# Kernel optimization log

Measured on AMD Instinct MI355X. Metric: run time of the kernel, lower is better.

Reference implementation:

```python
import jax, jax.numpy as jnp
import numpy as np

N_VAR, N_CON, N_SOC = 100_000, 100_000, 20_000
E_VC, E_SC = 2_000_000, 300_000
H = 64


def setup_inputs() -> dict:
    key = jax.random.key(0)
    ks = iter(jax.random.split(key, 64))

    def rn(shape, s=0.05):
        return jax.random.normal(next(ks), shape, jnp.float32) * s

    inp = {
        "var_x": rn((N_VAR, 7), 1.0),
        "con_x": rn((N_CON, 4), 1.0),
        "soc_x": rn((N_SOC, 6), 1.0),
        "W_var": rn((7, H)), "b_var": jnp.zeros((H,), jnp.float32),
        "W_con": rn((4, H)), "b_con": jnp.zeros((H,), jnp.float32),
        "W_soc": rn((6, H)), "b_soc": jnp.zeros((H,), jnp.float32),
    }
    for l in ("l1", "l2"):
        for d in ("f", "b"):
            inp[f"{l}{d}_Wp"] = rn((H, H))
            inp[f"{l}{d}_bp"] = jnp.zeros((H,), jnp.float32)
            inp[f"{l}{d}_Ws"] = rn((H, H))
            inp[f"{l}{d}_Wn"] = rn((H, H))
            inp[f"{l}{d}_b"] = jnp.zeros((H,), jnp.float32)
    inp["W_hid"] = rn((H, H)); inp["b_hid"] = jnp.zeros((H,), jnp.float32)
    inp["W_out"] = rn((H, 1)); inp["b_out"] = jnp.zeros((1,), jnp.float32)
    inp["vc_src"] = jax.random.randint(next(ks), (E_VC,), 0, N_VAR)
    inp["vc_dst"] = jax.random.randint(next(ks), (E_VC,), 0, N_CON)
    inp["sc_src"] = jax.random.randint(next(ks), (E_SC,), 0, N_SOC)
    inp["sc_dst"] = jax.random.randint(next(ks), (E_SC,), 0, N_CON)
    return inp


def _sage_pool(x_src, x_dst, src, dst, n_dst, Wp, bp, Ws, Wn, b):
    """DGL SAGEConv(aggregator_type='pool') on one bipartite relation.

    max-pool of relu(fc_pool(src feats)) over in-edges, then fc_self + fc_neigh + bias.
    """
    pooled = jax.nn.relu(x_src @ Wp + bp)                       # [N_src, H]
    agg = jax.ops.segment_max(pooled[src], dst, num_segments=n_dst)  # [N_dst, H]
    agg = jnp.where(jnp.isfinite(agg), agg, 0.0)                # zero in-degree -> 0 (DGL semantics)
    return x_dst @ Ws + agg @ Wn + b


def reference(var_x, con_x, soc_x,
              W_var, b_var, W_con, b_con, W_soc, b_soc,
              l1f_Wp, l1f_bp, l1f_Ws, l1f_Wn, l1f_b,
              l1b_Wp, l1b_bp, l1b_Ws, l1b_Wn, l1b_b,
              l2f_Wp, l2f_bp, l2f_Ws, l2f_Wn, l2f_b,
              l2b_Wp, l2b_bp, l2b_Ws, l2b_Wn, l2b_b,
              W_hid, b_hid, W_out, b_out,
              vc_src, vc_dst, sc_src, sc_dst):
    n_var, n_con, n_soc = var_x.shape[0], con_x.shape[0], soc_x.shape[0]

    # PreNormLayer with beta=0, sigma=1 (non-trainable, no pretrain update) is identity.
    h_var = jax.nn.relu(var_x @ W_var + b_var)
    h_con = jax.nn.relu(con_x @ W_con + b_con)
    h_soc = jax.nn.relu(soc_x @ W_soc + b_soc)

    # Each conv layer shares one SAGEConv for {v2c, s2c} and one for {c2v, c2s}.
    layers = [
        ((l1f_Wp, l1f_bp, l1f_Ws, l1f_Wn, l1f_b), (l1b_Wp, l1b_bp, l1b_Ws, l1b_Wn, l1b_b)),
        ((l2f_Wp, l2f_bp, l2f_Ws, l2f_Wn, l2f_b), (l2b_Wp, l2b_bp, l2b_Ws, l2b_Wn, l2b_b)),
    ]

    # n_passes = 1
    # forward half-pass: update constraint nodes; HeteroGraphConv sums v2c and s2c outputs.
    for fwd, _ in layers:
        c = (_sage_pool(h_var, h_con, vc_src, vc_dst, n_con, *fwd)
             + _sage_pool(h_soc, h_con, sc_src, sc_dst, n_con, *fwd))
        h_con = jax.nn.relu(c)
    # backward half-pass: update var and soc nodes from constraints (c2v, c2s = reversed edges).
    for _, bwd in layers:
        v = _sage_pool(h_con, h_var, vc_dst, vc_src, n_var, *bwd)
        s = _sage_pool(h_con, h_soc, sc_dst, sc_src, n_soc, *bwd)
        h_var = jax.nn.relu(v)
        h_soc = jax.nn.relu(s)

    # Output MLP: [Linear, ReLU]*2 in the source duplicates ONE shared Linear module.
    z = h_var
    for _ in range(2):
        z = jax.nn.relu(z @ W_hid + b_hid)
    return z @ W_out + b_out  # [n_var, 1] per-variable logits (readout_op=None)
```

## Files before the change

kernel.cpp:

```cpp
#include <hip/hip_runtime.h>

#define NV 100000
#define NC 100000
#define NSOC 20000
#define NVS (NV + NSOC)
#define EVC 2000000
#define ESC 300000
#define H 64

constexpr int BSH = 7;
constexpr int NBMAX = 1024;
constexpr int EPB = 8192;

template<int K1, int NSEC, bool RELU, int TR>
__global__ __launch_bounds__(256) void gemm_lds(
    const float* X1, const float* __restrict__ W1,
    const float* __restrict__ X2, const float* __restrict__ W2,
    const float* __restrict__ bias, float* out,
    int N, float s1)
{
  __shared__ __align__(16) float sx1[TR * K1];
  __shared__ __align__(16) float sx2[NSEC ? TR * H : 4];

  const int n0 = blockIdx.x * TR;

  if constexpr ((K1 & 3) == 0) {
    const float4* X4 = reinterpret_cast<const float4*>(X1);
    float4* S4 = reinterpret_cast<float4*>(sx1);
    const long base4 = (long)n0 * K1 / 4;
    const long lim4 = (long)N * K1 / 4;
    for (int i = threadIdx.x; i < TR * K1 / 4; i += 256)
      S4[i] = (base4 + i < lim4) ? X4[base4 + i] : make_float4(0.f, 0.f, 0.f, 0.f);
  } else {
    const long base = (long)n0 * K1;
    const long lim = (long)N * K1;
    for (int i = threadIdx.x; i < TR * K1; i += 256)
      sx1[i] = (base + i < lim) ? X1[base + i] : 0.f;
  }
  if constexpr (NSEC) {
    const float4* X4 = reinterpret_cast<const float4*>(X2);
    float4* S4 = reinterpret_cast<float4*>(sx2);
    const long base4 = (long)n0 * H / 4;
    const long lim4 = (long)N * H / 4;
    for (int i = threadIdx.x; i < TR * H / 4; i += 256)
      S4[i] = (base4 + i < lim4) ? X4[base4 + i] : make_float4(0.f, 0.f, 0.f, 0.f);
  }
  __syncthreads();

  const int lane = threadIdx.x & 63;
  const int wv = threadIdx.x >> 6;

  float w1[K1];
#pragma unroll
  for (int k = 0; k < K1; ++k) w1[k] = W1[k * H + lane];
  float w2[NSEC ? H : 1];
  if constexpr (NSEC) {
#pragma unroll
    for (int k = 0; k < H; ++k) w2[k] = W2[k * H + lane];
  }
  const float bj = bias[lane];

  constexpr int RPW = TR / 4;
  const int r0 = wv * RPW;

  if constexpr (K1 == H) {
    for (int i = 0; i < RPW; i += 2) {
      const int na = n0 + r0 + i;
      if (na >= N) break;
      const bool wb = (na + 1) < N;

      const float4* xa = reinterpret_cast<const float4*>(sx1 + (r0 + i) * H);
      const float4* xb = reinterpret_cast<const float4*>(sx1 + (r0 + i + 1) * H);
      float a0 = 0.f, a1 = 0.f, a2 = 0.f, a3 = 0.f;
      float b0 = 0.f, b1 = 0.f, b2 = 0.f, b3 = 0.f;
#pragma unroll
      for (int k4 = 0; k4 < H / 4; ++k4) {
        const float4 va = xa[k4];
        const float4 vb = xb[k4];
        a0 = fmaf(va.x, w1[4 * k4 + 0], a0);
        b0 = fmaf(vb.x, w1[4 * k4 + 0], b0);
        a1 = fmaf(va.y, w1[4 * k4 + 1], a1);
        b1 = fmaf(vb.y, w1[4 * k4 + 1], b1);
        a2 = fmaf(va.z, w1[4 * k4 + 2], a2);
        b2 = fmaf(vb.z, w1[4 * k4 + 2], b2);
        a3 = fmaf(va.w, w1[4 * k4 + 3], a3);
        b3 = fmaf(vb.w, w1[4 * k4 + 3], b3);
      }
      float accA = s1 * (((a0 + a1) + (a2 + a3)) + bj);
      float accB = s1 * (((b0 + b1) + (b2 + b3)) + bj);

      if constexpr (NSEC) {
        const float4* ya = reinterpret_cast<const float4*>(sx2 + (r0 + i) * H);
        const float4* yb = reinterpret_cast<const float4*>(sx2 + (r0 + i + 1) * H);
        a0 = 0.f; a1 = 0.f; a2 = 0.f; a3 = 0.f;
        b0 = 0.f; b1 = 0.f; b2 = 0.f; b3 = 0.f;
#pragma unroll
        for (int k4 = 0; k4 < H / 4; ++k4) {
          const float4 va = ya[k4];
          const float4 vb = yb[k4];
          a0 = fmaf(va.x, w2[4 * k4 + 0], a0);
          b0 = fmaf(vb.x, w2[4 * k4 + 0], b0);
          a1 = fmaf(va.y, w2[4 * k4 + 1], a1);
          b1 = fmaf(vb.y, w2[4 * k4 + 1], b1);
          a2 = fmaf(va.z, w2[4 * k4 + 2], a2);
          b2 = fmaf(vb.z, w2[4 * k4 + 2], b2);
          a3 = fmaf(va.w, w2[4 * k4 + 3], a3);
          b3 = fmaf(vb.w, w2[4 * k4 + 3], b3);
        }
        accA += (a0 + a1) + (a2 + a3);
        accB += (b0 + b1) + (b2 + b3);
      }

      if constexpr (RELU) { accA = fmaxf(accA, 0.f); accB = fmaxf(accB, 0.f); }
      out[(size_t)na * H + lane] = accA;
      if (wb) out[(size_t)(na + 1) * H + lane] = accB;
    }
  } else {
    for (int i = 0; i < RPW; i += 2) {
      const int na = n0 + r0 + i;
      if (na >= N) break;
      const bool wb = (na + 1) < N;
      const float* xa = sx1 + (r0 + i) * K1;
      const float* xb = sx1 + (r0 + i + 1) * K1;
      float accA = 0.f, accB = 0.f;
#pragma unroll
      for (int k = 0; k < K1; ++k) {
        accA = fmaf(xa[k], w1[k], accA);
        accB = fmaf(xb[k], w1[k], accB);
      }
      accA = s1 * (accA + bj);
      accB = s1 * (accB + bj);
      if constexpr (RELU) { accA = fmaxf(accA, 0.f); accB = fmaxf(accB, 0.f); }
      out[(size_t)na * H + lane] = accA;
      if (wb) out[(size_t)(na + 1) * H + lane] = accB;
    }
  }
}

template<int TR>
__global__ __launch_bounds__(256) void dualgemm_k(
    const float* __restrict__ X, const float* __restrict__ Wa,
    const float* __restrict__ ba, const float* __restrict__ Wb,
    const float* __restrict__ bb, float* __restrict__ out, int N)
{
  __shared__ __align__(16) float sx[TR * H];
  const int n0 = blockIdx.x * TR;
  {
    const float4* X4 = reinterpret_cast<const float4*>(X);
    float4* S4 = reinterpret_cast<float4*>(sx);
    const long base4 = (long)n0 * (H / 4);
    const long lim4 = (long)N * (H / 4);
    for (int i = threadIdx.x; i < TR * H / 4; i += 256)
      S4[i] = (base4 + i < lim4) ? X4[base4 + i] : make_float4(0.f, 0.f, 0.f, 0.f);
  }
  __syncthreads();

  const int lane = threadIdx.x & 63;
  const int wv = threadIdx.x >> 6;
  float wA[H], wB[H];
#pragma unroll
  for (int k = 0; k < H; ++k) { wA[k] = Wa[k * H + lane]; wB[k] = Wb[k * H + lane]; }
  const float bja = ba[lane];
  const float bjb = bb[lane];

  constexpr int RPW = TR / 4;
  const int r0 = wv * RPW;
  for (int i = 0; i < RPW; i += 2) {
    const int na = n0 + r0 + i;
    if (na >= N) break;
    const bool hasB = (na + 1) < N;

    const float4* xa = reinterpret_cast<const float4*>(sx + (r0 + i) * H);
    const float4* xb = reinterpret_cast<const float4*>(sx + (r0 + i + 1) * H);
    float pa0 = 0.f, pa1 = 0.f, pa2 = 0.f, pa3 = 0.f;
    float pb0 = 0.f, pb1 = 0.f, pb2 = 0.f, pb3 = 0.f;
    float qa0 = 0.f, qa1 = 0.f, qa2 = 0.f, qa3 = 0.f;
    float qb0 = 0.f, qb1 = 0.f, qb2 = 0.f, qb3 = 0.f;
#pragma unroll
    for (int k4 = 0; k4 < H / 4; ++k4) {
      const float4 va = xa[k4];
      const float4 vb = xb[k4];
      pa0 = fmaf(va.x, wA[4 * k4 + 0], pa0);
      pb0 = fmaf(vb.x, wA[4 * k4 + 0], pb0);
      qa0 = fmaf(va.x, wB[4 * k4 + 0], qa0);
      qb0 = fmaf(vb.x, wB[4 * k4 + 0], qb0);
      pa1 = fmaf(va.y, wA[4 * k4 + 1], pa1);
      pb1 = fmaf(vb.y, wA[4 * k4 + 1], pb1);
      qa1 = fmaf(va.y, wB[4 * k4 + 1], qa1);
      qb1 = fmaf(vb.y, wB[4 * k4 + 1], qb1);
      pa2 = fmaf(va.z, wA[4 * k4 + 2], pa2);
      pb2 = fmaf(vb.z, wA[4 * k4 + 2], pb2);
      qa2 = fmaf(va.z, wB[4 * k4 + 2], qa2);
      qb2 = fmaf(vb.z, wB[4 * k4 + 2], qb2);
      pa3 = fmaf(va.w, wA[4 * k4 + 3], pa3);
      pb3 = fmaf(vb.w, wA[4 * k4 + 3], pb3);
      qa3 = fmaf(va.w, wB[4 * k4 + 3], qa3);
      qb3 = fmaf(vb.w, wB[4 * k4 + 3], qb3);
    }
    const float accAa = fmaxf((pa0 + pa1) + (pa2 + pa3) + bja, 0.f);
    const float accAb = fmaxf((qa0 + qa1) + (qa2 + qa3) + bjb, 0.f);
    out[(size_t)na * 128 + lane] = accAa;
    out[(size_t)na * 128 + 64 + lane] = accAb;
    if (hasB) {
      const float accBa = fmaxf((pb0 + pb1) + (pb2 + pb3) + bja, 0.f);
      const float accBb = fmaxf((qb0 + qb1) + (qb2 + qb3) + bjb, 0.f);
      out[(size_t)(na + 1) * 128 + lane] = accBa;
      out[(size_t)(na + 1) * 128 + 64 + lane] = accBb;
    }
  }
}

template<int TR>
__global__ __launch_bounds__(256) void mlp_k(
    const float* __restrict__ X, const float* __restrict__ W,
    const float* __restrict__ bh, const float* __restrict__ Wout,
    const float* __restrict__ bo, float* __restrict__ out, int N)
{
  __shared__ __align__(16) float sx[TR * H];
  __shared__ __align__(16) float sz[4][H];

  const int n0 = blockIdx.x * TR;
  {
    const float4* X4 = reinterpret_cast<const float4*>(X);
    float4* S4 = reinterpret_cast<float4*>(sx);
    const long base4 = (long)n0 * H / 4;
    const long lim4 = (long)N * H / 4;
    for (int i = threadIdx.x; i < TR * H / 4; i += 256)
      S4[i] = (base4 + i < lim4) ? X4[base4 + i] : make_float4(0.f, 0.f, 0.f, 0.f);
  }
  __syncthreads();

  const int lane = threadIdx.x & 63;
  const int wv = threadIdx.x >> 6;
  float w[H];
#pragma unroll
  for (int k = 0; k < H; ++k) w[k] = W[k * H + lane];
  const float bhl = bh[lane];
  const float wo = Wout[lane];
  const float bol = bo[0];

  constexpr int RPW = TR / 4;
  const int r0 = wv * RPW;
  for (int i = 0; i < RPW; ++i) {
    const int n = n0 + r0 + i;
    if (n >= N) break;
    const float4* x4 = reinterpret_cast<const float4*>(sx + (r0 + i) * H);
    float a0 = 0.f, a1 = 0.f, a2 = 0.f, a3 = 0.f;
#pragma unroll
    for (int k4 = 0; k4 < H / 4; ++k4) {
      const float4 v = x4[k4];
      a0 = fmaf(v.x, w[4 * k4 + 0], a0);
      a1 = fmaf(v.y, w[4 * k4 + 1], a1);
      a2 = fmaf(v.z, w[4 * k4 + 2], a2);
      a3 = fmaf(v.w, w[4 * k4 + 3], a3);
    }
    const float z1 = fmaxf((a0 + a1) + (a2 + a3) + bhl, 0.f);
    sz[wv][lane] = z1;
    const float4* z4 = reinterpret_cast<const float4*>(sz[wv]);
    a0 = 0.f; a1 = 0.f; a2 = 0.f; a3 = 0.f;
#pragma unroll
    for (int k4 = 0; k4 < H / 4; ++k4) {
      const float4 v = z4[k4];
      a0 = fmaf(v.x, w[4 * k4 + 0], a0);
      a1 = fmaf(v.y, w[4 * k4 + 1], a1);
      a2 = fmaf(v.z, w[4 * k4 + 2], a2);
      a3 = fmaf(v.w, w[4 * k4 + 3], a3);
    }
    const float z2 = fmaxf((a0 + a1) + (a2 + a3) + bhl, 0.f);
    float v = z2 * wo;
#pragma unroll
    for (int off = 32; off; off >>= 1) v += __shfl_down(v, off);
    if (lane == 0) out[n] = v + bol;
  }
}

__global__ __launch_bounds__(256) void bhist_k(const int* __restrict__ key,
                                               int* __restrict__ bcnt, int E, int nb) {
  __shared__ int h[NBMAX];
  for (int i = threadIdx.x; i < nb; i += 256) h[i] = 0;
  __syncthreads();
  const int base = blockIdx.x * EPB;
  for (int i = threadIdx.x; i < EPB; i += 256) {
    const int e = base + i;
    if (e < E) atomicAdd(&h[key[e] >> BSH], 1);
  }
  __syncthreads();
  for (int i = threadIdx.x; i < nb; i += 256)
    if (h[i]) atomicAdd(&bcnt[i], h[i]);
}

__global__ __launch_bounds__(1024) void bscan_k(const int* __restrict__ bcnt,
                                                int* __restrict__ bcur,
                                                int* __restrict__ sbase, int nb) {
  __shared__ int s[1024];
  const int t = threadIdx.x;
  const int v = (t < nb) ? bcnt[t] : 0;
  s[t] = v;
  __syncthreads();
  for (int off = 1; off < 1024; off <<= 1) {
    int x = (t >= off) ? s[t - off] : 0;
    __syncthreads();
    s[t] += x;
    __syncthreads();
  }
  if (t < nb) {
    const int ex = s[t] - v;
    bcur[t] = ex;
    sbase[t] = ex;
    if (t == nb - 1) sbase[nb] = s[t];
  }
}

__global__ __launch_bounds__(256) void bscatter_k(
    const int* __restrict__ key, const int* __restrict__ payload,
    int* __restrict__ bcur, int2* __restrict__ sorted, int E, int nb) {
  __shared__ int h[NBMAX];
  __shared__ int gb[NBMAX];
  __shared__ unsigned short lr[EPB];
  for (int i = threadIdx.x; i < nb; i += 256) h[i] = 0;
  __syncthreads();
  const int base = blockIdx.x * EPB;
  for (int i = threadIdx.x; i < EPB; i += 256) {
    const int e = base + i;
    if (e < E) lr[i] = (unsigned short)atomicAdd(&h[key[e] >> BSH], 1);
  }
  __syncthreads();
  for (int i = threadIdx.x; i < nb; i += 256)
    if (h[i]) gb[i] = atomicAdd(&bcur[i], h[i]);
  __syncthreads();
  for (int i = threadIdx.x; i < EPB; i += 256) {
    const int e = base + i;
    if (e < E) {
      const int k = key[e];
      sorted[gb[k >> BSH] + lr[i]] = make_int2(k, payload[e]);
    }
  }
}

__global__ __launch_bounds__(256) void bfinish_k(
    const int2* __restrict__ sorted, const int* __restrict__ sbase,
    int* __restrict__ rp, int* __restrict__ ei, int Nn) {
  __shared__ int cnt[128];
// ... 74 lines not shown
  m.w = fmaxf(m.w, __shfl_xor(m.w, 32));
  return m;
}

__global__ __launch_bounds__(256) void gather2f_k(
    const float4* __restrict__ t4,
    const int* __restrict__ rpCv, const int* __restrict__ eiCv,
    const int* __restrict__ rpCs, const int* __restrict__ eiCs,
    float4* __restrict__ agg1, float4* __restrict__ agg2, int N)
{
  const int lane = threadIdx.x & 63;
  const int g = lane >> 5, sub = lane & 31;
  const int n = __builtin_amdgcn_readfirstlane(blockIdx.x * 4 + (threadIdx.x >> 6));
  if (n >= N) return;
  const float4 a = gmax2_csr(t4, rpCv, eiCv, n, g, sub);
  const float4 b = gmax2_csr(t4 + (size_t)NV * 32, rpCs, eiCs, n, g, sub);
  const float4 r = make_float4(a.x + b.x, a.y + b.y, a.z + b.z, a.w + b.w);
  if (g == 0) {
    if (sub < 16) agg1[(size_t)n * 16 + sub] = r;
    else          agg2[(size_t)n * 16 + (sub - 16)] = r;
  }
}

__global__ __launch_bounds__(256) void gathervs2_k(
    const float4* __restrict__ t4,
    const int* __restrict__ rpV, const int* __restrict__ eiV,
    const int* __restrict__ rpS, const int* __restrict__ eiS,
    float4* __restrict__ agg1, float4* __restrict__ agg2)
{
  const int lane = threadIdx.x & 63;
  const int g = lane >> 5, sub = lane & 31;
  const int n = __builtin_amdgcn_readfirstlane(blockIdx.x * 4 + (threadIdx.x >> 6));
  if (n >= NVS) return;
  float4 m;
  if (n < NV) m = gmax2_csr(t4, rpV, eiV, n, g, sub);
  else        m = gmax2_csr(t4, rpS, eiS, n - NV, g, sub);
  if (g == 0) {
    if (sub < 16) agg1[(size_t)n * 16 + sub] = m;
    else          agg2[(size_t)n * 16 + (sub - 16)] = m;
  }
}

extern "C" void kernel_launch(void* const* d_in, const int* in_sizes, int n_in,
                              void* d_out, int out_size, void* d_ws, size_t ws_size,
                              hipStream_t stream) {
  const float* var_x = (const float*)d_in[0];
  const float* con_x = (const float*)d_in[1];
  const float* soc_x = (const float*)d_in[2];
  const float* W_var = (const float*)d_in[3];
  const float* b_var = (const float*)d_in[4];
  const float* W_con = (const float*)d_in[5];
  const float* b_con = (const float*)d_in[6];
  const float* W_soc = (const float*)d_in[7];
  const float* b_soc = (const float*)d_in[8];
  const float* L[4][5];
  for (int l = 0; l < 4; ++l)
    for (int p = 0; p < 5; ++p)
      L[l][p] = (const float*)d_in[9 + l * 5 + p];
  const float* W_hid = (const float*)d_in[29];
  const float* b_hid = (const float*)d_in[30];
  const float* W_out = (const float*)d_in[31];
  const float* b_out = (const float*)d_in[32];
  const int* vc_src = (const int*)d_in[33];
  const int* vc_dst = (const int*)d_in[34];
  const int* sc_src = (const int*)d_in[35];
  const int* sc_dst = (const int*)d_in[36];

  char* ws = (char*)d_ws;
  const size_t F_VS = (size_t)NVS * H * 4;
  const size_t F_C  = (size_t)NC * H * 4;
  float* hvs   = (float*)(ws);
  float* h_con = (float*)(ws + F_VS);
  float* bufA  = (float*)(ws + F_VS + F_C);
  float* bufB  = (float*)(ws + 3 * F_VS + F_C);
  int2*  sorted = (int2*)bufB;
  char* csr = ws + 3 * F_VS + 3 * F_C;
  int* rpCv = (int*)(csr);
  int* eiCv = rpCv + (NC + 1);
  int* rpCs = eiCv + EVC;
  int* eiCs = rpCs + (NC + 1);
  int* rpV  = eiCs + ESC;
  int* eiV  = rpV + (NV + 1);
  int* rpS  = eiV + EVC;
  int* eiS  = rpS + (NSOC + 1);
  int* aux  = eiS + ESC;
  int* bcnt[4];
  for (int i = 0; i < 4; ++i) bcnt[i] = aux + i * 1024;
  int* bcur  = aux + 4 * 1024;
  int* sbase = aux + 5 * 1024;

  constexpr int TR = 64;
  auto grid_l = [](int n) { return dim3((unsigned)((n + TR - 1) / TR)); };
  auto grid_w = [](int n) { return dim3((unsigned)((n + 3) / 4)); };
  auto grid_b = [](int e) { return dim3((unsigned)((e + EPB - 1) / EPB)); };
  const dim3 B(256);

  float* h_var = hvs;
  float* h_soc = hvs + (size_t)NV * H;

  hipMemsetAsync(aux, 0, 4 * 1024 * sizeof(int), stream);

  auto build_csr = [&](const int* key, const int* payload, int E, int Nn,
                       int* rp, int* ei, int bi) {
    const int nb = (Nn + (1 << BSH) - 1) >> BSH;
    bhist_k<<<grid_b(E), B, 0, stream>>>(key, bcnt[bi], E, nb);
    bscan_k<<<dim3(1), dim3(1024), 0, stream>>>(bcnt[bi], bcur, sbase, nb);
    bscatter_k<<<grid_b(E), B, 0, stream>>>(key, payload, bcur, sorted, E, nb);
    bfinish_k<<<dim3((unsigned)nb), B, 0, stream>>>(sorted, sbase, rp, ei, Nn);
  };

  build_csr(vc_dst, vc_src, EVC, NC, rpCv, eiCv, 0);
  build_csr(sc_dst, sc_src, ESC, NC, rpCs, eiCs, 1);
  build_csr(vc_src, vc_dst, EVC, NV, rpV, eiV, 2);
  build_csr(sc_src, sc_dst, ESC, NSOC, rpS, eiS, 3);

  gemm_lds<7, 0, true, TR><<<grid_l(NV), B, 0, stream>>>(var_x, W_var, nullptr, nullptr, b_var, h_var, NV, 1.f);
  gemm_lds<4, 0, true, TR><<<grid_l(NC), B, 0, stream>>>(con_x, W_con, nullptr, nullptr, b_con, h_con, NC, 1.f);
  gemm_lds<6, 0, true, TR><<<grid_l(NSOC), B, 0, stream>>>(soc_x, W_soc, nullptr, nullptr, b_soc, h_soc, NSOC, 1.f);

  float* agg1f = bufB;
  float* agg2f = bufB + (size_t)NC * H;
  dualgemm_k<TR><<<grid_l(NVS), B, 0, stream>>>(hvs, L[0][0], L[0][1], L[2][0], L[2][1], bufA, NVS);
  gather2f_k<<<grid_w(NC), B, 0, stream>>>((const float4*)bufA, rpCv, eiCv, rpCs, eiCs,
                                           (float4*)agg1f, (float4*)agg2f, NC);
  gemm_lds<64, 1, true, TR><<<grid_l(NC), B, 0, stream>>>(h_con, L[0][2], agg1f, L[0][3], L[0][4], h_con, NC, 2.f);
  gemm_lds<64, 1, true, TR><<<grid_l(NC), B, 0, stream>>>(h_con, L[2][2], agg2f, L[2][3], L[2][4], h_con, NC, 2.f);

  float* agg1b = bufA;
  float* agg2b = bufA + (size_t)NVS * H;
  dualgemm_k<TR><<<grid_l(NC), B, 0, stream>>>(h_con, L[1][0], L[1][1], L[3][0], L[3][1], bufB, NC);
  gathervs2_k<<<grid_w(NVS), B, 0, stream>>>((const float4*)bufB, rpV, eiV, rpS, eiS,
                                             (float4*)agg1b, (float4*)agg2b);
  gemm_lds<64, 1, true, TR><<<grid_l(NVS), B, 0, stream>>>(hvs, L[1][2], agg1b, L[1][3], L[1][4], hvs, NVS, 1.f);
  gemm_lds<64, 1, true, TR><<<grid_l(NVS), B, 0, stream>>>(hvs, L[3][2], agg2b, L[3][3], L[3][4], hvs, NVS, 1.f);

  mlp_k<TR><<<grid_l(NV), B, 0, stream>>>(hvs, W_hid, b_hid, W_out, b_out, (float*)d_out, NV);
}
```

Measured before the change: 832.6 us.

## Fuse embedding, layer updates and MLP into per-tile kernels; skip soc backward path

Replaces the separate GEMM launches with fused per-tile kernels. Embedding and both pool projections run in one kernel; the constraint embedding, both forward updates and the backward pool projections run in another; the variable updates and output MLP run in a third, keeping intermediates in LDS instead of global memory. It drops the soc-node backward update entirely, since the output depends only on var nodes. It also merges the two vc CSR builds into one histogram/scan/scatter pass. This cuts global traffic and launch count at the price of more registers and LDS per block, which may reduce occupancy.

```diff
diff --git a/kernel.cpp b/kernel.cpp
--- a/kernel.cpp
+++ b/kernel.cpp
@@ -11,273 +11,293 @@
 constexpr int BSH = 7;
 constexpr int NBMAX = 1024;
 constexpr int EPB = 8192;
-
-template<int K1, int NSEC, bool RELU, int TR>
-__global__ __launch_bounds__(256) void gemm_lds(
-    const float* X1, const float* __restrict__ W1,
-    const float* __restrict__ X2, const float* __restrict__ W2,
-    const float* __restrict__ bias, float* out,
-    int N, float s1)
-{
-  __shared__ __align__(16) float sx1[TR * K1];
-  __shared__ __align__(16) float sx2[NSEC ? TR * H : 4];
-
-  const int n0 = blockIdx.x * TR;
-
-  if constexpr ((K1 & 3) == 0) {
-    const float4* X4 = reinterpret_cast<const float4*>(X1);
-    float4* S4 = reinterpret_cast<float4*>(sx1);
-    const long base4 = (long)n0 * K1 / 4;
-    const long lim4 = (long)N * K1 / 4;
-    for (int i = threadIdx.x; i < TR * K1 / 4; i += 256)
-      S4[i] = (base4 + i < lim4) ? X4[base4 + i] : make_float4(0.f, 0.f, 0.f, 0.f);
-  } else {
-    const long base = (long)n0 * K1;
-    const long lim = (long)N * K1;
-    for (int i = threadIdx.x; i < TR * K1; i += 256)
-      sx1[i] = (base + i < lim) ? X1[base + i] : 0.f;
-  }
-  if constexpr (NSEC) {
-    const float4* X4 = reinterpret_cast<const float4*>(X2);
-    float4* S4 = reinterpret_cast<float4*>(sx2);
-    const long base4 = (long)n0 * H / 4;
-    const long lim4 = (long)N * H / 4;
-    for (int i = threadIdx.x; i < TR * H / 4; i += 256)
-      S4[i] = (base4 + i < lim4) ? X4[base4 + i] : make_float4(0.f, 0.f, 0.f, 0.f);
-  }
-  __syncthreads();
-
-  const int lane = threadIdx.x & 63;
-  const int wv = threadIdx.x >> 6;
-
-  float w1[K1];
-#pragma unroll
-  for (int k = 0; k < K1; ++k) w1[k] = W1[k * H + lane];
-  float w2[NSEC ? H : 1];
-  if constexpr (NSEC) {
-#pragma unroll
-    for (int k = 0; k < H; ++k) w2[k] = W2[k * H + lane];
-  }
+constexpr int TR = 64;
+
+__device__ __forceinline__ void stage_tile(const float* __restrict__ X, float* s,
+                                           int n0, int N, int tid) {
+  const float4* X4 = reinterpret_cast<const float4*>(X);
+  float4* S4 = reinterpret_cast<float4*>(s);
+  const long base4 = (long)n0 * (H / 4);
+  const long lim4 = (long)N * (H / 4);
+  for (int i = tid; i < TR * H / 4; i += 256)
+    S4[i] = (base4 + i < lim4) ? X4[base4 + i] : make_float4(0.f, 0.f, 0.f, 0.f);
+}
+
+__device__ __forceinline__ void apply_layer_inplace(
+    float* sh, const float* sa,
+    const float* __restrict__ Wself, const float* __restrict__ Wneigh,
+    const float* __restrict__ bias, int lane, int r0, float s1)
+{
+  float ws[H], wn[H];
+#pragma unroll
+  for (int k = 0; k < H; ++k) ws[k] = Wself[k * H + lane];
+#pragma unroll
+  for (int k = 0; k < H; ++k) wn[k] = Wneigh[k * H + lane];
   const float bj = bias[lane];
-
-  constexpr int RPW = TR / 4;
-  const int r0 = wv * RPW;
-
-  if constexpr (K1 == H) {
-    for (int i = 0; i < RPW; i += 2) {
-      const int na = n0 + r0 + i;
-      if (na >= N) break;
-      const bool wb = (na + 1) < N;
-
-      const float4* xa = reinterpret_cast<const float4*>(sx1 + (r0 + i) * H);
-      const float4* xb = reinterpret_cast<const float4*>(sx1 + (r0 + i + 1) * H);
-      float a0 = 0.f, a1 = 0.f, a2 = 0.f, a3 = 0.f;
-      float b0 = 0.f, b1 = 0.f, b2 = 0.f, b3 = 0.f;
-#pragma unroll
-      for (int k4 = 0; k4 < H / 4; ++k4) {
-        const float4 va = xa[k4];
-        const float4 vb = xb[k4];
-        a0 = fmaf(va.x, w1[4 * k4 + 0], a0);
-        b0 = fmaf(vb.x, w1[4 * k4 + 0], b0);
-        a1 = fmaf(va.y, w1[4 * k4 + 1], a1);
-        b1 = fmaf(vb.y, w1[4 * k4 + 1], b1);
-        a2 = fmaf(va.z, w1[4 * k4 + 2], a2);
-        b2 = fmaf(vb.z, w1[4 * k4 + 2], b2);
-        a3 = fmaf(va.w, w1[4 * k4 + 3], a3);
-        b3 = fmaf(vb.w, w1[4 * k4 + 3], b3);
-      }
-      float accA = s1 * (((a0 + a1) + (a2 + a3)) + bj);
-      float accB = s1 * (((b0 + b1) + (b2 + b3)) + bj);
-
-      if constexpr (NSEC) {
-        const float4* ya = reinterpret_cast<const float4*>(sx2 + (r0 + i) * H);
-        const float4* yb = reinterpret_cast<const float4*>(sx2 + (r0 + i + 1) * H);
-        a0 = 0.f; a1 = 0.f; a2 = 0.f; a3 = 0.f;
-        b0 = 0.f; b1 = 0.f; b2 = 0.f; b3 = 0.f;
-#pragma unroll
-        for (int k4 = 0; k4 < H / 4; ++k4) {
-          const float4 va = ya[k4];
-          const float4 vb = yb[k4];
-          a0 = fmaf(va.x, w2[4 * k4 + 0], a0);
-          b0 = fmaf(vb.x, w2[4 * k4 + 0], b0);
-          a1 = fmaf(va.y, w2[4 * k4 + 1], a1);
-          b1 = fmaf(vb.y, w2[4 * k4 + 1], b1);
-          a2 = fmaf(va.z, w2[4 * k4 + 2], a2);
-          b2 = fmaf(vb.z, w2[4 * k4 + 2], b2);
-          a3 = fmaf(va.w, w2[4 * k4 + 3], a3);
-          b3 = fmaf(vb.w, w2[4 * k4 + 3], b3);
-        }
-        accA += (a0 + a1) + (a2 + a3);
-        accB += (b0 + b1) + (b2 + b3);
-      }
-
-      if constexpr (RELU) { accA = fmaxf(accA, 0.f); accB = fmaxf(accB, 0.f); }
-      out[(size_t)na * H + lane] = accA;
-      if (wb) out[(size_t)(na + 1) * H + lane] = accB;
-    }
-  } else {
-    for (int i = 0; i < RPW; i += 2) {
-      const int na = n0 + r0 + i;
-      if (na >= N) break;
-      const bool wb = (na + 1) < N;
-      const float* xa = sx1 + (r0 + i) * K1;
-      const float* xb = sx1 + (r0 + i + 1) * K1;
-      float accA = 0.f, accB = 0.f;
-#pragma unroll
-      for (int k = 0; k < K1; ++k) {
-        accA = fmaf(xa[k], w1[k], accA);
-        accB = fmaf(xb[k], w1[k], accB);
-      }
-      accA = s1 * (accA + bj);
-      accB = s1 * (accB + bj);
-      if constexpr (RELU) { accA = fmaxf(accA, 0.f); accB = fmaxf(accB, 0.f); }
-      out[(size_t)na * H + lane] = accA;
-      if (wb) out[(size_t)(na + 1) * H + lane] = accB;
-    }
-  }
-}
-
-template<int TR>
-__global__ __launch_bounds__(256) void dualgemm_k(
-    const float* __restrict__ X, const float* __restrict__ Wa,
-    const float* __restrict__ ba, const float* __restrict__ Wb,
-    const float* __restrict__ bb, float* __restrict__ out, int N)
-{
-  __shared__ __align__(16) float sx[TR * H];
+  for (int i = 0; i < 16; i += 2) {
+    const float4* xa = reinterpret_cast<const float4*>(sh + (r0 + i) * H);
+    const float4* xb = reinterpret_cast<const float4*>(sh + (r0 + i + 1) * H);
+    float a0 = 0.f, a1 = 0.f, a2 = 0.f, a3 = 0.f;
+    float b0 = 0.f, b1 = 0.f, b2 = 0.f, b3 = 0.f;
+#pragma unroll
+    for (int k4 = 0; k4 < H / 4; ++k4) {
+      const float4 va = xa[k4], vb = xb[k4];
+      a0 = fmaf(va.x, ws[4 * k4 + 0], a0); b0 = fmaf(vb.x, ws[4 * k4 + 0], b0);
+      a1 = fmaf(va.y, ws[4 * k4 + 1], a1); b1 = fmaf(vb.y, ws[4 * k4 + 1], b1);
+      a2 = fmaf(va.z, ws[4 * k4 + 2], a2); b2 = fmaf(vb.z, ws[4 * k4 + 2], b2);
+      a3 = fmaf(va.w, ws[4 * k4 + 3], a3); b3 = fmaf(vb.w, ws[4 * k4 + 3], b3);
+    }
+    float accA = s1 * (((a0 + a1) + (a2 + a3)) + bj);
+    float accB = s1 * (((b0 + b1) + (b2 + b3)) + bj);
+    const float4* ya = reinterpret_cast<const float4*>(sa + (r0 + i) * H);
+    const float4* yb = reinterpret_cast<const float4*>(sa + (r0 + i + 1) * H);
+    a0 = 0.f; a1 = 0.f; a2 = 0.f; a3 = 0.f;
+    b0 = 0.f; b1 = 0.f; b2 = 0.f; b3 = 0.f;
+#pragma unroll
+    for (int k4 = 0; k4 < H / 4; ++k4) {
+      const float4 va = ya[k4], vb = yb[k4];
+      a0 = fmaf(va.x, wn[4 * k4 + 0], a0); b0 = fmaf(vb.x, wn[4 * k4 + 0], b0);
+      a1 = fmaf(va.y, wn[4 * k4 + 1], a1); b1 = fmaf(vb.y, wn[4 * k4 + 1], b1);
+      a2 = fmaf(va.z, wn[4 * k4 + 2], a2); b2 = fmaf(vb.z, wn[4 * k4 + 2], b2);
+      a3 = fmaf(va.w, wn[4 * k4 + 3], a3); b3 = fmaf(vb.w, wn[4 * k4 + 3], b3);
+    }
+    accA += (a0 + a1) + (a2 + a3);
+    accB += (b0 + b1) + (b2 + b3);
+    sh[(r0 + i) * H + lane] = fmaxf(accA, 0.f);
+    sh[(r0 + i + 1) * H + lane] = fmaxf(accB, 0.f);
+  }
+}
+
+__device__ __forceinline__ void apply_lin_inplace(
+    float* sh, const float* __restrict__ W, const float* __restrict__ b,
+    int lane, int r0)
+{
+  float w[H];
+#pragma unroll
+  for (int k = 0; k < H; ++k) w[k] = W[k * H + lane];
+  const float bj = b[lane];
+  for (int i = 0; i < 16; i += 2) {
+    const float4* xa = reinterpret_cast<const float4*>(sh + (r0 + i) * H);
+    const float4* xb = reinterpret_cast<const float4*>(sh + (r0 + i + 1) * H);
+    float a0 = 0.f, a1 = 0.f, a2 = 0.f, a3 = 0.f;
+    float b0 = 0.f, b1 = 0.f, b2 = 0.f, b3 = 0.f;
+#pragma unroll
+    for (int k4 = 0; k4 < H / 4; ++k4) {
+      const float4 va = xa[k4], vb = xb[k4];
+      a0 = fmaf(va.x, w[4 * k4 + 0], a0); b0 = fmaf(vb.x, w[4 * k4 + 0], b0);
+      a1 = fmaf(va.y, w[4 * k4 + 1], a1); b1 = fmaf(vb.y, w[4 * k4 + 1], b1);
+      a2 = fmaf(va.z, w[4 * k4 + 2], a2); b2 = fmaf(vb.z, w[4 * k4 + 2], b2);
+      a3 = fmaf(va.w, w[4 * k4 + 3], a3); b3 = fmaf(vb.w, w[4 * k4 + 3], b3);
+    }
+    sh[(r0 + i) * H + lane] = fmaxf((a0 + a1) + (a2 + a3) + bj, 0.f);
+    sh[(r0 + i + 1) * H + lane] = fmaxf((b0 + b1) + (b2 + b3) + bj, 0.f);
+  }
+}
+
+__device__ __forceinline__ void apply_pool_out(
+    const float* sh, const float* __restrict__ Wp, const float* __restrict__ bp,
+    int lane, int r0, int n0, int N, float* __restrict__ pooled, int colOff)
+{
+  float w[H];
+#pragma unroll
+  for (int k = 0; k < H; ++k) w[k] = Wp[k * H + lane];
+  const float bj = bp[lane];
+  for (int i = 0; i < 16; i += 2) {
+    const float4* xa = reinterpret_cast<const float4*>(sh + (r0 + i) * H);
+    const float4* xb = reinterpret_cast<const float4*>(sh + (r0 + i + 1) * H);
+    float a0 = 0.f, a1 = 0.f, a2 = 0.f, a3 = 0.f;
+    float b0 = 0.f, b1 = 0.f, b2 = 0.f, b3 = 0.f;
+#pragma unroll
+    for (int k4 = 0; k4 < H / 4; ++k4) {
+      const float4 va = xa[k4], vb = xb[k4];
+      a0 = fmaf(va.x, w[4 * k4 + 0], a0); b0 = fmaf(vb.x, w[4 * k4 + 0], b0);
+      a1 = fmaf(va.y, w[4 * k4 + 1], a1); b1 = fmaf(vb.y, w[4 * k4 + 1], b1);
+      a2 = fmaf(va.z, w[4 * k4 + 2], a2); b2 = fmaf(vb.z, w[4 * k4 + 2], b2);
+      a3 = fmaf(va.w, w[4 * k4 + 3], a3); b3 = fmaf(vb.w, w[4 * k4 + 3], b3);
+    }
+    const int na = n0 + r0 + i;
+    if (na < N)
+      pooled[(size_t)na * 128 + colOff + lane] =
+          fmaxf((a0 + a1) + (a2 + a3) + bj, 0.f);
+    if (na + 1 < N)
+      pooled[(size_t)(na + 1) * 128 + colOff + lane] =
+          fmaxf((b0 + b1) + (b2 + b3) + bj, 0.f);
+  }
+}
+
+template<int K, bool WRITEH>
+__global__ __launch_bounds__(256) void emb_pool_k(
+    const float* __restrict__ X, const float* __restrict__ We,
+    const float* __restrict__ be,
+    const float* __restrict__ Wp1, const float* __restrict__ bp1,
+    const float* __restrict__ Wp2, const float* __restrict__ bp2,
+    float* __restrict__ h_out, float* __restrict__ pooled, int N)
+{
+  __shared__ __align__(16) float sxe[TR * K];
+  __shared__ __align__(16) float sh[TR * H];
   const int n0 = blockIdx.x * TR;
   {
-    const float4* X4 = reinterpret_cast<const float4*>(X);
-    float4* S4 = reinterpret_cast<float4*>(sx);
-    const long base4 = (long)n0 * (H / 4);
-    const long lim4 = (long)N * (H / 4);
-    for (int i = threadIdx.x; i < TR * H / 4; i += 256)
-      S4[i] = (base4 + i < lim4) ? X4[base4 + i] : make_float4(0.f, 0.f, 0.f, 0.f);
-  }
-  __syncthreads();
-
+    const long base = (long)n0 * K, lim = (long)N * K;
+    for (int i = threadIdx.x; i < TR * K; i += 256)
+      sxe[i] = (base + i < lim) ? X[base + i] : 0.f;
+  }
+  __syncthreads();
   const int lane = threadIdx.x & 63;
-  const int wv = threadIdx.x >> 6;
-  float wA[H], wB[H];
-#pragma unroll
-  for (int k = 0; k < H; ++k) { wA[k] = Wa[k * H + lane]; wB[k] = Wb[k * H + lane]; }
-  const float bja = ba[lane];
-  const float bjb = bb[lane];
-
-  constexpr int RPW = TR / 4;
-  const int r0 = wv * RPW;
-  for (int i = 0; i < RPW; i += 2) {
-    const int na = n0 + r0 + i;
-    if (na >= N) break;
-    const bool hasB = (na + 1) < N;
-
-    const float4* xa = reinterpret_cast<const float4*>(sx + (r0 + i) * H);
-    const float4* xb = reinterpret_cast<const float4*>(sx + (r0 + i + 1) * H);
-    float pa0 = 0.f, pa1 = 0.f, pa2 = 0.f, pa3 = 0.f;
-    float pb0 = 0.f, pb1 = 0.f, pb2 = 0.f, pb3 = 0.f;
-    float qa0 = 0.f, qa1 = 0.f, qa2 = 0.f, qa3 = 0.f;
-    float qb0 = 0.f, qb1 = 0.f, qb2 = 0.f, qb3 = 0.f;
-#pragma unroll
-    for (int k4 = 0; k4 < H / 4; ++k4) {
-      const float4 va = xa[k4];
-      const float4 vb = xb[k4];
-      pa0 = fmaf(va.x, wA[4 * k4 + 0], pa0);
-      pb0 = fmaf(vb.x, wA[4 * k4 + 0], pb0);
-      qa0 = fmaf(va.x, wB[4 * k4 + 0], qa0);
-      qb0 = fmaf(vb.x, wB[4 * k4 + 0], qb0);
-      pa1 = fmaf(va.y, wA[4 * k4 + 1], pa1);
-      pb1 = fmaf(vb.y, wA[4 * k4 + 1], pb1);
-      qa1 = fmaf(va.y, wB[4 * k4 + 1], qa1);
-      qb1 = fmaf(vb.y, wB[4 * k4 + 1], qb1);
-      pa2 = fmaf(va.z, wA[4 * k4 + 2], pa2);
-      pb2 = fmaf(vb.z, wA[4 * k4 + 2], pb2);
-      qa2 = fmaf(va.z, wB[4 * k4 + 2], qa2);
-      qb2 = fmaf(vb.z, wB[4 * k4 + 2], qb2);
-      pa3 = fmaf(va.w, wA[4 * k4 + 3], pa3);
-      pb3 = fmaf(vb.w, wA[4 * k4 + 3], pb3);
-      qa3 = fmaf(va.w, wB[4 * k4 + 3], qa3);
-      qb3 = fmaf(vb.w, wB[4 * k4 + 3], qb3);
-    }
-    const float accAa = fmaxf((pa0 + pa1) + (pa2 + pa3) + bja, 0.f);
-    const float accAb = fmaxf((qa0 + qa1) + (qa2 + qa3) + bjb, 0.f);
-    out[(size_t)na * 128 + lane] = accAa;
-    out[(size_t)na * 128 + 64 + lane] = accAb;
-    if (hasB) {
-      const float accBa = fmaxf((pb0 + pb1) + (pb2 + pb3) + bja, 0.f);
-      const float accBb = fmaxf((qb0 + qb1) + (qb2 + qb3) + bjb, 0.f);
-      out[(size_t)(na + 1) * 128 + lane] = accBa;
-      out[(size_t)(na + 1) * 128 + 64 + lane] = accBb;
-    }
-  }
-}
-
-template<int TR>
-__global__ __launch_bounds__(256) void mlp_k(
-    const float* __restrict__ X, const float* __restrict__ W,
-    const float* __restrict__ bh, const float* __restrict__ Wout,
-    const float* __restrict__ bo, float* __restrict__ out, int N)
-{
-  __shared__ __align__(16) float sx[TR * H];
-  __shared__ __align__(16) float sz[4][H];
-
+  const int r0 = (threadIdx.x >> 6) * 16;
+  {
+    float w[K];
+#pragma unroll
+    for (int k = 0; k < K; ++k) w[k] = We[k * H + lane];
+    const float bj = be[lane];
+    for (int i = 0; i < 16; i += 2) {
+      const float* xa = sxe + (r0 + i) * K;
+      const float* xb = sxe + (r0 + i + 1) * K;
+      float a = 0.f, b = 0.f;
+#pragma unroll
+      for (int k = 0; k < K; ++k) { a = fmaf(xa[k], w[k], a); b = fmaf(xb[k], w[k], b); }
+      a = fmaxf(a + bj, 0.f);
+      b = fmaxf(b + bj, 0.f);
+      sh[(r0 + i) * H + lane] = a;
+      sh[(r0 + i + 1) * H + lane] = b;
+      if constexpr (WRITEH) {
+        const int na = n0 + r0 + i;
+        if (na < N) h_out[(size_t)na * H + lane] = a;
+        if (na + 1 < N) h_out[(size_t)(na + 1) * H + lane] = b;
+      }
+    }
+  }
+  __syncthreads();
+  apply_pool_out(sh, Wp1, bp1, lane, r0, n0, N, pooled, 0);
+  __syncthreads();
+  apply_pool_out(sh, Wp2, bp2, lane, r0, n0, N, pooled, 64);
+}
+
+__global__ __launch_bounds__(256) void con_update_k(
+    const float* __restrict__ con_x, const float* __restrict__ We,
+    const float* __restrict__ be,
+    const float* __restrict__ Ws1, const float* __restrict__ Wn1, const float* __restrict__ b1,
+    const float* __restrict__ Ws2, const float* __restrict__ Wn2, const float* __restrict__ b2,
+    const float* __restrict__ Wp1, const float* __restrict__ bp1,
+    const float* __restrict__ Wp2, const float* __restrict__ bp2,
+    const float* __restrict__ agg1, const float* __restrict__ agg2,
+    float* __restrict__ pooledB, int N)
+{
+  __shared__ __align__(16) float sh[TR * H];
+  __shared__ __align__(16) float sa1[TR * H];
+  __shared__ __align__(16) float sa2[TR * H];
+  __shared__ __align__(16) float sxe[TR * 4];
   const int n0 = blockIdx.x * TR;
   {
-    const float4* X4 = reinterpret_cast<const float4*>(X);
-    float4* S4 = reinterpret_cast<float4*>(sx);
-    const long base4 = (long)n0 * H / 4;
-    const long lim4 = (long)N * H / 4;
-    for (int i = threadIdx.x; i < TR * H / 4; i += 256)
-      S4[i] = (base4 + i < lim4) ? X4[base4 + i] : make_float4(0.f, 0.f, 0.f, 0.f);
-  }
-  __syncthreads();
-
+    const float4* X4 = reinterpret_cast<const float4*>(con_x);
+    float4* S4 = reinterpret_cast<float4*>(sxe);
+    for (int i = threadIdx.x; i < TR; i += 256)
+      S4[i] = (n0 + i < N) ? X4[n0 + i] : make_float4(0.f, 0.f, 0.f, 0.f);
+  }
+  stage_tile(agg1, sa1, n0, N, threadIdx.x);
+  stage_tile(agg2, sa2, n0, N, threadIdx.x);
+  __syncthreads();
   const int lane = threadIdx.x & 63;
-  const int wv = threadIdx.x >> 6;
-  float w[H];
-#pragma unroll
-  for (int k = 0; k < H; ++k) w[k] = W[k * H + lane];
-  const float bhl = bh[lane];
-  const float wo = Wout[lane];
-  const float bol = bo[0];
-
-  constexpr int RPW = TR / 4;
-  const int r0 = wv * RPW;
-  for (int i = 0; i < RPW; ++i) {
-    const int n = n0 + r0 + i;
-    if (n >= N) break;
-    const float4* x4 = reinterpret_cast<const float4*>(sx + (r0 + i) * H);
-    float a0 = 0.f, a1 = 0.f, a2 = 0.f, a3 = 0.f;
-#pragma unroll
-    for (int k4 = 0; k4 < H / 4; ++k4) {
-      const float4 v = x4[k4];
-      a0 = fmaf(v.x, w[4 * k4 + 0], a0);
-      a1 = fmaf(v.y, w[4 * k4 + 1], a1);
-      a2 = fmaf(v.z, w[4 * k4 + 2], a2);
-      a3 = fmaf(v.w, w[4 * k4 + 3], a3);
-    }
-    const float z1 = fmaxf((a0 + a1) + (a2 + a3) + bhl, 0.f);
-    sz[wv][lane] = z1;
-    const float4* z4 = reinterpret_cast<const float4*>(sz[wv]);
-    a0 = 0.f; a1 = 0.f; a2 = 0.f; a3 = 0.f;
-#pragma unroll
-    for (int k4 = 0; k4 < H / 4; ++k4) {
-      const float4 v = z4[k4];
-      a0 = fmaf(v.x, w[4 * k4 + 0], a0);
-      a1 = fmaf(v.y, w[4 * k4 + 1], a1);
-      a2 = fmaf(v.z, w[4 * k4 + 2], a2);
-      a3 = fmaf(v.w, w[4 * k4 + 3], a3);
-    }
-    const float z2 = fmaxf((a0 + a1) + (a2 + a3) + bhl, 0.f);
-    float v = z2 * wo;
-#pragma unroll
-    for (int off = 32; off; off >>= 1) v += __shfl_down(v, off);
-    if (lane == 0) out[n] = v + bol;
-  }
+  const int r0 = (threadIdx.x >> 6) * 16;
+  {
+    float w[4];
+#pragma unroll
+    for (int k = 0; k < 4; ++k) w[k] = We[k * H + lane];
+    const float bj = be[lane];
+    for (int i = 0; i < 16; ++i) {
+      const float* x = sxe + (r0 + i) * 4;
+      float a = 0.f;
+#pragma unroll
+      for (int k = 0; k < 4; ++k) a = fmaf(x[k], w[k], a);
+      sh[(r0 + i) * H + lane] = fmaxf(a + bj, 0.f);
+    }
+  }
+  __syncthreads();
+  apply_layer_inplace(sh, sa1, Ws1, Wn1, b1, lane, r0, 2.f);
+  __syncthreads();
+  apply_layer_inplace(sh, sa2, Ws2, Wn2, b2, lane, r0, 2.f);
+  __syncthreads();
+  apply_pool_out(sh, Wp1, bp1, lane, r0, n0, N, pooledB, 0);
+  __syncthreads();
+  apply_pool_out(sh, Wp2, bp2, lane, r0, n0, N, pooledB, 64);
+}
+
+__global__ __launch_bounds__(256) void var_update_mlp_k(
+    const float* __restrict__ hv,
+    const float* __restrict__ Ws1, const float* __restrict__ Wn1, const float* __restrict__ b1,
+    const float* __restrict__ Ws2, const float* __restrict__ Wn2, const float* __restrict__ b2,
+    const float* __restrict__ Wh, const float* __restrict__ bh,
+    const float* __restrict__ Wo, const float* __restrict__ bo,
+    const float* __restrict__ agg1, const float* __restrict__ agg2,
+    float* __restrict__ out, int N)
+{
+  __shared__ __align__(16) float sh[TR * H];
+  __shared__ __align__(16) float sa1[TR * H];
+  __shared__ __align__(16) float sa2[TR * H];
+  const int n0 = blockIdx.x * TR;
+  stage_tile(hv, sh, n0, N, threadIdx.x);
+  stage_tile(agg1, sa1, n0, N, threadIdx.x);
+  stage_tile(agg2, sa2, n0, N, threadIdx.x);
+  __syncthreads();
+  const int lane = threadIdx.x & 63;
+  const int r0 = (threadIdx.x >> 6) * 16;
+  apply_layer_inplace(sh, sa1, Ws1, Wn1, b1, lane, r0, 1.f);
+  __syncthreads();
+  apply_layer_inplace(sh, sa2, Ws2, Wn2, b2, lane, r0, 1.f);
+  __syncthreads();
+  apply_lin_inplace(sh, Wh, bh, lane, r0);
+  __syncthreads();
+  {
+    float w[H];
+#pragma unroll
+    for (int k = 0; k < H; ++k) w[k] = Wh[k * H + lane];
+    const float bhl = bh[lane];
+    const float wo = Wo[lane];
+    const float bol = bo[0];
+    for (int i = 0; i < 16; ++i) {
+      const int n = n0 + r0 + i;
+      const float4* x4 = reinterpret_cast<const float4*>(sh + (r0 + i) * H);
+      float a0 = 0.f, a1 = 0.f, a2 = 0.f, a3 = 0.f;
+#pragma unroll
+      for (int k4 = 0; k4 < H / 4; ++k4) {
+        const float4 v = x4[k4];
+        a0 = fmaf(v.x, w[4 * k4 + 0], a0);
+        a1 = fmaf(v.y, w[4 * k4 + 1], a1);
+        a2 = fmaf(v.z, w[4 * k4 + 2], a2);
+        a3 = fmaf(v.w, w[4 * k4 + 3], a3);
+      }
+      const float z2 = fmaxf((a0 + a1) + (a2 + a3) + bhl, 0.f);
+      float v = z2 * wo;
+#pragma unroll
+      for (int off = 32; off; off >>= 1) v += __shfl_down(v, off);
+      if (lane == 0 && n < N) out[n] = v + bol;
+    }
+  }
+}
+
+__global__ __launch_bounds__(256) void bhist2_k(
+    const int* __restrict__ kD, const int* __restrict__ kS,
+    int* __restrict__ bcntD, int* __restrict__ bcntS, int E, int nbD, int nbS)
+{
+  __shared__ int hD[NBMAX], hS[NBMAX];
+  for (int i = threadIdx.x; i < NBMAX; i += 256) { hD[i] = 0; hS[i] = 0; }
+  __syncthreads();
+  const int base = blockIdx.x * EPB;
+  for (int i = threadIdx.x; i < EPB; i += 256) {
+    const int e = base + i;
+    if (e < E) {
+      atomicAdd(&hD[kD[e] >> BSH], 1);
+      atomicAdd(&hS[kS[e] >> BSH], 1);
+    }
+  }
+  __syncthreads();
+  for (int i = threadIdx.x; i < nbD; i += 256) if (hD[i]) atomicAdd(&bcntD[i], hD[i]);
+  for (int i = threadIdx.x; i < nbS; i += 256) if (hS[i]) atomicAdd(&bcntS[i], hS[i]);
 }
 
 __global__ __launch_bounds__(256) void bhist_k(const int* __restrict__ key,
                                                int* __restrict__ bcnt, int E, int nb) {
   __shared__ int h[NBMAX];
-  for (int i = threadIdx.x; i < nb; i += 256) h[i] = 0;
+  for (int i = threadIdx.x; i < NBMAX; i += 256) h[i] = 0;
   __syncthreads();
   const int base = blockIdx.x * EPB;
   for (int i = threadIdx.x; i < EPB; i += 256) {
@@ -289,12 +309,11 @@
     if (h[i]) atomicAdd(&bcnt[i], h[i]);
 }
 
-__global__ __launch_bounds__(1024) void bscan_k(const int* __restrict__ bcnt,
-                                                int* __restrict__ bcur,
-                                                int* __restrict__ sbase, int nb) {
-  __shared__ int s[1024];
+__device__ __forceinline__ void scan_dev(const int* __restrict__ cnt,
+                                         int* __restrict__ cur,
+                                         int* __restrict__ sbase, int nb, int* s) {
   const int t = threadIdx.x;
-  const int v = (t < nb) ? bcnt[t] : 0;
+  const int v = (t < nb) ? cnt[t] : 0;
   s[t] = v;
   __syncthreads();
   for (int off = 1; off < 1024; off <<= 1) {
@@ -305,9 +324,55 @@
   }
   if (t < nb) {
     const int ex = s[t] - v;
-    bcur[t] = ex;
+    cur[t] = ex;
     sbase[t] = ex;
     if (t == nb - 1) sbase[nb] = s[t];
+  }
+  __syncthreads();
+}
+
+__global__ __launch_bounds__(1024) void bscan2_k(
+    const int* __restrict__ cD, int* __restrict__ curD, int* __restrict__ sbD, int nbD,
+    const int* __restrict__ cS, int* __restrict__ curS, int* __restrict__ sbS, int nbS) {
+  __shared__ int s[1024];
+  scan_dev(cD, curD, sbD, nbD, s);
+  scan_dev(cS, curS, sbS, nbS, s);
+}
+
+__global__ __launch_bounds__(1024) void bscan1_k(
+    const int* __restrict__ c, int* __restrict__ cur, int* __restrict__ sb, int nb) {
+  __shared__ int s[1024];
+  scan_dev(c, cur, sb, nb, s);
+}
+
+__global__ __launch_bounds__(256) void bscatter2_k(
+    const int* __restrict__ kD, const int* __restrict__ kS,
+    int* __restrict__ bcurD, int* __restrict__ bcurS,
+    int2* __restrict__ sortedD, int2* __restrict__ sortedS, int E, int nbD, int nbS)
+{
+  __shared__ int hD[NBMAX], gbD[NBMAX], hS[NBMAX], gbS[NBMAX];
+  __shared__ unsigned short lrD[EPB], lrS[EPB];
+  for (int i = threadIdx.x; i < NBMAX; i += 256) { hD[i] = 0; hS[i] = 0; }
+  __syncthreads();
+  const int base = blockIdx.x * EPB;
+  for (int i = threadIdx.x; i < EPB; i += 256) {
+    const int e = base + i;
+    if (e < E) {
+      lrD[i] = (unsigned short)atomicAdd(&hD[kD[e] >> BSH], 1);
+      lrS[i] = (unsigned short)atomicAdd(&hS[kS[e] >> BSH], 1);
+    }
+  }
+  __syncthreads();
+  for (int i = threadIdx.x; i < nbD; i += 256) if (hD[i]) gbD[i] = atomicAdd(&bcurD[i], hD[i]);
+  for (int i = threadIdx.x; i < nbS; i += 256) if (hS[i]) gbS[i] = atomicAdd(&bcurS[i], hS[i]);
+  __syncthreads();
+  for (int i = threadIdx.x; i < EPB; i += 256) {
+    const int e = base + i;
+    if (e < E) {
+      const int d = kD[e], s = kS[e];
+      sortedD[gbD[d >> BSH] + lrD[i]] = make_int2(d, s);
+      sortedS[gbS[s >> BSH] + lrS[i]] = make_int2(s, d);
+    }
   }
 }
 
@@ -317,7 +382,7 @@
   __shared__ int h[NBMAX];
   __shared__ int gb[NBMAX];
   __shared__ unsigned short lr[EPB];
-  for (int i = threadIdx.x; i < nb; i += 256) h[i] = 0;
+  for (int i = threadIdx.x; i < NBMAX; i += 256) h[i] = 0;
   __syncthreads();
   const int base = blockIdx.x * EPB;
   for (int i = threadIdx.x; i < EPB; i += 256) {
@@ -438,19 +503,16 @@
   }
 }
 
-__global__ __launch_bounds__(256) void gathervs2_k(
+__global__ __launch_bounds__(256) void gatherB_k(
     const float4* __restrict__ t4,
-    const int* __restrict__ rpV, const int* __restrict__ eiV,
-    const int* __restrict__ rpS, const int* __restrict__ eiS,
-    float4* __restrict__ agg1, float4* __restrict__ agg2)
+    const int* __restrict__ rp, const int* __restrict__ ei,
+    float4* __restrict__ agg1, float4* __restrict__ agg2, int N)
 {
   const int lane = threadIdx.x & 63;
   const int g = lane >> 5, sub = lane & 31;
   const int n = __builtin_amdgcn_readfirstlane(blockIdx.x * 4 + (threadIdx.x >> 6));
-  if (n >= NVS) return;
-  float4 m;
-  if (n < NV) m = gmax2_csr(t4, rpV, eiV, n, g, sub);
-  else        m = gmax2_csr(t4, rpS, eiS, n - NV, g, sub);
+  if (n >= N) return;
+  const float4 m = gmax2_csr(t4, rp, ei, n, g, sub);
   if (g == 0) {
     if (sub < 16) agg1[(size_t)n * 16 + sub] = m;
     else          agg2[(size_t)n * 16 + (sub - 16)] = m;
@@ -483,72 +545,78 @@
   const int* sc_dst = (const int*)d_in[36];
 
   char* ws = (char*)d_ws;
-  const size_t F_VS = (size_t)NVS * H * 4;
-  const size_t F_C  = (size_t)NC * H * 4;
-  float* hvs   = (float*)(ws);
-  float* h_con = (float*)(ws + F_VS);
-  float* bufA  = (float*)(ws + F_VS + F_C);
-  float* bufB  = (float*)(ws + 3 * F_VS + F_C);
-  int2*  sorted = (int2*)bufB;
-  char* csr = ws + 3 * F_VS + 3 * F_C;
-  int* rpCv = (int*)(csr);
+  const size_t SZ_HV = (size_t)NV * H * 4;
+  const size_t SZ_PF = (size_t)NVS * 128 * 4;
+  const size_t SZ_AF = 2ull * NC * H * 4;
+  const size_t SZ_PB = (size_t)NC * 128 * 4;
+  float* h_var   = (float*)ws;
+  float* pooledF = (float*)(ws + SZ_HV);
+  float* agg1b   = pooledF;
+  float* agg2b   = pooledF + (size_t)NV * H;
+  float* agg1f   = (float*)(ws + SZ_HV + SZ_PF);
+  float* agg2f   = agg1f + (size_t)NC * H;
+  int2*  sortedD = (int2*)agg1f;
+  int2*  sortedS = (int2*)((char*)agg1f + (size_t)EVC * 8);
+  float* pooledB = (float*)(ws + SZ_HV + SZ_PF + SZ_AF);
+  int* csr = (int*)(ws + SZ_HV + SZ_PF + SZ_AF + SZ_PB);
+  int* rpCv = csr;
   int* eiCv = rpCv + (NC + 1);
   int* rpCs = eiCv + EVC;
   int* eiCs = rpCs + (NC + 1);
   int* rpV  = eiCs + ESC;
   int* eiV  = rpV + (NV + 1);
-  int* rpS  = eiV + EVC;
-  int* eiS  = rpS + (NSOC + 1);
-  int* aux  = eiS + ESC;
-  int* bcnt[4];
-  for (int i = 0; i < 4; ++i) bcnt[i] = aux + i * 1024;
-  int* bcur  = aux + 4 * 1024;
-  int* sbase = aux + 5 * 1024;
-
-  constexpr int TR = 64;
+  int* aux  = eiV + EVC;
+  int* bcntD = aux;
+  int* bcntS = aux + 1024;
+  int* bcntC = aux + 2048;
+  int* bcurD = aux + 3072;
+  int* bcurS = aux + 4096;
+  int* bcurC = aux + 5120;
+  int* sbD   = aux + 6144;
+  int* sbS   = sbD + 1056;
+  int* sbC   = sbS + 1056;
+
+  const int nbC = (NC + 127) >> BSH;
+  const int nbV = (NV + 127) >> BSH;
   auto grid_l = [](int n) { return dim3((unsigned)((n + TR - 1) / TR)); };
   auto grid_w = [](int n) { return dim3((unsigned)((n + 3) / 4)); };
   auto grid_b = [](int e) { return dim3((unsigned)((e + EPB - 1) / EPB)); };
   const dim3 B(256);
 
-  float* h_var = hvs;
-  float* h_soc = hvs + (size_t)NV * H;
-
-  hipMemsetAsync(aux, 0, 4 * 1024 * sizeof(int), stream);
-
-  auto build_csr = [&](const int* key, const int* payload, int E, int Nn,
-                       int* rp, int* ei, int bi) {
-    const int nb = (Nn + (1 << BSH) - 1) >> BSH;
-    bhist_k<<<grid_b(E), B, 0, stream>>>(key, bcnt[bi], E, nb);
-    bscan_k<<<dim3(1), dim3(1024), 0, stream>>>(bcnt[bi], bcur, sbase, nb);
-    bscatter_k<<<grid_b(E), B, 0, stream>>>(key, payload, bcur, sorted, E, nb);
-    bfinish_k<<<dim3((unsigned)nb), B, 0, stream>>>(sorted, sbase, rp, ei, Nn);
-  };
-
-  build_csr(vc_dst, vc_src, EVC, NC, rpCv, eiCv, 0);
-  build_csr(sc_dst, sc_src, ESC, NC, rpCs, eiCs, 1);
-  build_csr(vc_src, vc_dst, EVC, NV, rpV, eiV, 2);
-  build_csr(sc_src, sc_dst, ESC, NSOC, rpS, eiS, 3);
-
-  gemm_lds<7, 0, true, TR><<<grid_l(NV), B, 0, stream>>>(var_x, W_var, nullptr, nullptr, b_var, h_var, NV, 1.f);
-  gemm_lds<4, 0, true, TR><<<grid_l(NC), B, 0, stream>>>(con_x, W_con, nullptr, nullptr, b_con, h_con, NC, 1.f);
-  gemm_lds<6, 0, true, TR><<<grid_l(NSOC), B, 0, stream>>>(soc_x, W_soc, nullptr, nullptr, b_soc, h_soc, NSOC, 1.f);
-
-  float* agg1f = bufB;
-  float* agg2f = bufB + (size_t)NC * H;
-  dualgemm_k<TR><<<grid_l(NVS), B, 0, stream>>>(hvs, L[0][0], L[0][1], L[2][0], L[2][1], bufA, NVS);
-  gather2f_k<<<grid_w(NC), B, 0, stream>>>((const float4*)bufA, rpCv, eiCv, rpCs, eiCs,
-                                           (float4*)agg1f, (float4*)agg2f, NC);
-  gemm_lds<64, 1, true, TR><<<grid_l(NC), B, 0, stream>>>(h_con, L[0][2], agg1f, L[0][3], L[0][4], h_con, NC, 2.f);
-  gemm_lds<64, 1, true, TR><<<grid_l(NC), B, 0, stream>>>(h_con, L[2][2], agg2f, L[2][3], L[2][4], h_con, NC, 2.f);
-
-  float* agg1b = bufA;
-  float* agg2b = bufA + (size_t)NVS * H;
-  dualgemm_k<TR><<<grid_l(NC), B, 0, stream>>>(h_con, L[1][0], L[1][1], L[3][0], L[3][1], bufB, NC);
-  gathervs2_k<<<grid_w(NVS), B, 0, stream>>>((const float4*)bufB, rpV, eiV, rpS, eiS,
-                                             (float4*)agg1b, (float4*)agg2b);
-  gemm_lds<64, 1, true, TR><<<grid_l(NVS), B, 0, stream>>>(hvs, L[1][2], agg1b, L[1][3], L[1][4], hvs, NVS, 1.f);
-  gemm_lds<64, 1, true, TR><<<grid_l(NVS), B, 0, stream>>>(hvs, L[3][2], agg2b, L[3][3], L[3][4], hvs, NVS, 1.f);
-
-  mlp_k<TR><<<grid_l(NV), B, 0, stream>>>(hvs, W_hid, b_hid, W_out, b_out, (float*)d_out, NV);
-}
+  hipMemsetAsync(aux, 0, 3072 * sizeof(int), stream);
+
+  bhist2_k<<<grid_b(EVC), B, 0, stream>>>(vc_dst, vc_src, bcntD, bcntS, EVC, nbC, nbV);
+  bscan2_k<<<dim3(1), dim3(1024), 0, stream>>>(bcntD, bcurD, sbD, nbC, bcntS, bcurS, sbS, nbV);
+  bscatter2_k<<<grid_b(EVC), B, 0, stream>>>(vc_dst, vc_src, bcurD, bcurS, sortedD, sortedS, EVC, nbC, nbV);
+  bfinish_k<<<dim3((unsigned)nbC), B, 0, stream>>>(sortedD, sbD, rpCv, eiCv, NC);
+  bfinish_k<<<dim3((unsigned)nbV), B, 0, stream>>>(sortedS, sbS, rpV, eiV, NV);
+  bhist_k<<<grid_b(ESC), B, 0, stream>>>(sc_dst, bcntC, ESC, nbC);
+  bscan1_k<<<dim3(1), dim3(1024), 0, stream>>>(bcntC, bcurC, sbC, nbC);
+  bscatter_k<<<grid_b(ESC), B, 0, stream>>>(sc_dst, sc_src, bcurC, sortedD, ESC, nbC);
+  bfinish_k<<<dim3((unsigned)nbC), B, 0, stream>>>(sortedD, sbC, rpCs, eiCs, NC);
+
+  emb_pool_k<7, true><<<grid_l(NV), B, 0, stream>>>(
+      var_x, W_var, b_var, L[0][0], L[0][1], L[2][0], L[2][1], h_var, pooledF, NV);
+  emb_pool_k<6, false><<<grid_l(NSOC), B, 0, stream>>>(
+      soc_x, W_soc, b_soc, L[0][0], L[0][1], L[2][0], L[2][1], nullptr,
+      pooledF + (size_t)NV * 128, NSOC);
+
+  gather2f_k<<<grid_w(NC), B, 0, stream>>>(
+      (const float4*)pooledF, rpCv, eiCv, rpCs, eiCs,
+      (float4*)agg1f, (float4*)agg2f, NC);
+
+  con_update_k<<<grid_l(NC), B, 0, stream>>>(
+      con_x, W_con, b_con,
+      L[0][2], L[0][3], L[0][4], L[2][2], L[2][3], L[2][4],
+      L[1][0], L[1][1], L[3][0], L[3][1],
+      agg1f, agg2f, pooledB, NC);
+
+  gatherB_k<<<grid_w(NV), B, 0, stream>>>(
+      (const float4*)pooledB, rpV, eiV, (float4*)agg1b, (float4*)agg2b, NV);
+
+  var_update_mlp_k<<<grid_l(NV), B, 0, stream>>>(
+      h_var,
+      L[1][2], L[1][3], L[1][4], L[3][2], L[3][3], L[3][4],
+      W_hid, b_hid, W_out, b_out,
+      agg1b, agg2b, (float*)d_out, NV);
+}
```

Result: slower. 1.006 ms (+20.9%).
